# Performance work log

Hardware: AMD Instinct MI355X
Metric: run time of the kernel (lower is better)

## Reference

```python
import jax, jax.numpy as jnp
import numpy as np

B, S, D = 4, 2048, 1024
H, HD = 16, 64  # n_heads, head_dim (n_kv_heads == n_heads -> n_rep = 1)
WINDOW = 256
ROPE_THETA = 10000.0


def setup_inputs() -> dict:
    key = jax.random.key(0)
    ks = jax.random.split(key, 5)
    x = jax.random.normal(ks[0], (B, S, D), dtype=jnp.float32)
    scale = 0.02
    wq = jax.random.normal(ks[1], (D, D), dtype=jnp.float32) * scale
    wk = jax.random.normal(ks[2], (D, D), dtype=jnp.float32) * scale
    wv = jax.random.normal(ks[3], (D, D), dtype=jnp.float32) * scale
    wo = jax.random.normal(ks[4], (D, D), dtype=jnp.float32) * scale
    # RoPE frequencies: freqs_cis[t, i] = exp(1j * t / theta^(2i/HD)), i in [0, HD/2)
    inv_freq = 1.0 / (ROPE_THETA ** (jnp.arange(0, HD, 2, dtype=jnp.float32) / HD))
    t = jnp.arange(S, dtype=jnp.float32)
    ang = t[:, None] * inv_freq[None, :]  # [S, HD/2]
    return {"x": x, "freqs_cos": jnp.cos(ang), "freqs_sin": jnp.sin(ang),
            "wq": wq, "wk": wk, "wv": wv, "wo": wo}


def _apply_rope(xq, xk, cos, sin):
    # xq/xk: [B, S, H, HD]; cos/sin: [S, HD/2] broadcast as [1, S, 1, HD/2]
    def rot(v):
        vr = v.reshape(*v.shape[:-1], HD // 2, 2)
        v0, v1 = vr[..., 0], vr[..., 1]
        c = cos[None, :, None, :]
        s = sin[None, :, None, :]
        o0 = v0 * c - v1 * s
        o1 = v0 * s + v1 * c
        return jnp.stack([o0, o1], axis=-1).reshape(v.shape)
    return rot(xq), rot(xk)


def reference(x, freqs_cos, freqs_sin, wq, wk, wv, wo):
    b, s, _ = x.shape
    xq = (x @ wq.T).reshape(b, s, H, HD)
    xk = (x @ wk.T).reshape(b, s, H, HD)
    xv = (x @ wv.T).reshape(b, s, H, HD)
    xq, xk = _apply_rope(xq, xk, freqs_cos, freqs_sin)
    # [B, H, S, S] scores
    scores = jnp.einsum('bqhd,bkhd->bhqk', xq, xk) / jnp.sqrt(jnp.float32(HD))
    pos = jnp.arange(s)
    # masked (disallowed) when j > i (future) or i - j >= window
    bad = (pos[None, :] > pos[:, None]) | (pos[:, None] - pos[None, :] >= WINDOW)
    scores = jnp.where(bad[None, None], -jnp.inf, scores)
    attn = jax.nn.softmax(scores.astype(jnp.float32), axis=-1).astype(xq.dtype)
    out = jnp.einsum('bhqk,bkhd->bqhd', attn, xv).reshape(b, s, H * HD)
    return out @ wo.T
```

## Files before the change

### kernel.cpp

```cpp
#include <hip/hip_runtime.h>
#include <hip/hip_bf16.h>


typedef __bf16 bf16_t;
typedef __attribute__((ext_vector_type(8))) __bf16 bf16x8;
typedef __attribute__((ext_vector_type(4))) __bf16 bf16x4;
typedef __attribute__((ext_vector_type(4))) float f32x4;

#define MFMA16(a, b, c) __builtin_amdgcn_mfma_f32_16x16x32_bf16((a), (b), (c), 0, 0, 0)

__device__ __forceinline__ void async16(const void* g, void* l) {
    __builtin_amdgcn_global_load_lds(
        (const __attribute__((address_space(1))) unsigned int*)g,
        (__attribute__((address_space(3))) unsigned int*)l, 16, 0, 0);
}

#define BAR() do { asm volatile("" ::: "memory"); __builtin_amdgcn_s_barrier(); \
                   asm volatile("" ::: "memory"); } while (0)
#define VMC(N) asm volatile("s_waitcnt vmcnt(" #N ")" ::: "memory")

__global__ __launch_bounds__(256) void cvt_all(const float* __restrict__ x,
                                               const float* __restrict__ wq,
                                               const float* __restrict__ wk,
                                               const float* __restrict__ wv,
                                               const float* __restrict__ wo,
                                               bf16_t* __restrict__ xbf,
                                               bf16_t* __restrict__ wqkv,
                                               bf16_t* __restrict__ wobf) {
    const int blk = blockIdx.x;
    const float* s;
    bf16_t* d;
    int base;
    if (blk < 4096)      { s = x;  d = xbf;            base = blk; }
    else if (blk < 4608) { s = wq; d = wqkv;           base = blk - 4096; }
    else if (blk < 5120) { s = wk; d = wqkv + 1048576; base = blk - 4608; }
    else if (blk < 5632) { s = wv; d = wqkv + 2097152; base = blk - 5120; }
    else                 { s = wo; d = wobf;           base = blk - 5632; }
    const int i = (base * 256 + threadIdx.x) * 8;
    float4 a = *(const float4*)(s + i);
    float4 b = *(const float4*)(s + i + 4);
    bf16x8 o;
    o[0] = (bf16_t)a.x; o[1] = (bf16_t)a.y; o[2] = (bf16_t)a.z; o[3] = (bf16_t)a.w;
    o[4] = (bf16_t)b.x; o[5] = (bf16_t)b.y; o[6] = (bf16_t)b.z; o[7] = (bf16_t)b.w;
    *(bf16x8*)(d + i) = o;
}

template <typename OUT>
__global__ __launch_bounds__(512, 1) __attribute__((amdgpu_waves_per_eu(2)))
void gemm192(const bf16_t* __restrict__ A, const bf16_t* __restrict__ Bw,
             OUT* __restrict__ C, int M, int N, int K) {
    __shared__ __attribute__((aligned(16))) bf16_t As[32768];
    __shared__ __attribute__((aligned(16))) bf16_t Bs[24576];
    const int tid = threadIdx.x;
    const int l = tid & 63, w = tid >> 6;
    const int lr = l & 15, lg = l >> 4;
    const int wr = w >> 2, wc = w & 3;

    const int nwg = gridDim.x * gridDim.y;
    const int flat = blockIdx.y * gridDim.x + blockIdx.x;
    const int swz = (flat & 7) * (nwg >> 3) + (flat >> 3);
    const int bx = swz % gridDim.x, by = swz / gridDim.x;
    const long m0 = (long)by * 256, n0 = (long)bx * 192;
    const int NT = K >> 6;
    const int NI = NT >> 1;

    const int p  = w * 1024 + l * 16;
    const int pp = p ^ (((p >> 9) & 1) << 5);
    const int st = pp >> 10;
    const int rSt = (st >> 1) * 16 + ((pp >> 6) & 15);
    const int cSt = (st & 1) * 32 + ((pp >> 4) & 3) * 8;
    const bf16_t* aS = A  + (m0 + rSt) * K + cSt;
    const bf16_t* bS = Bw + (n0 + rSt) * K + cSt;
    const long uK = 64L * K;

    auto stageA = [&](int b, int u, int t) {
        async16(aS + (long)u * uK + (long)t * 64,
                (char*)As + b * 32768 + u * 8192 + w * 1024);
    };
    auto stageB = [&](int b, int u, int t) {
        async16(bS + (long)u * uK + (long)t * 64,
                (char*)Bs + b * 24576 + u * 8192 + w * 1024);
    };

    f32x4 acc[8][3] = {};
    bf16x8 afX[4], afY[4], bfX[3], bfY[3];
    const int swd = (lr & 8) << 2;

    auto loadAF = [&](int b, int mh, int ks, bf16x8 (&dst)[4]) {
#pragma unroll
        for (int mi = 0; mi < 4; ++mi) {
            const int off = (wr * 2 + mh) * 8192 + (mi * 2 + ks) * 1024 +
                            lr * 64 + lg * 16;
            dst[mi] = *(const bf16x8*)((const char*)As + b * 32768 + (off ^ swd));
        }
    };
    auto loadBF = [&](int b, int ks, bf16x8 (&dst)[3]) {
#pragma unroll
        for (int nj = 0; nj < 3; ++nj) {
            const int rg = wc * 48 + nj * 16 + lr;
            const int off = (rg >> 6) * 8192 + (((rg >> 4) & 3) * 2 + ks) * 1024 +
                            lr * 64 + lg * 16;
            dst[nj] = *(const bf16x8*)((const char*)Bs + b * 24576 + (off ^ swd));
        }
    };

#define QMM(MH, AF, BF) do {                                                   \
    __builtin_amdgcn_s_setprio(1);                                             \
    _Pragma("unroll")                                                          \
    for (int mi = 0; mi < 4; ++mi)                                             \
        _Pragma("unroll")                                                      \
        for (int nj = 0; nj < 3; ++nj)                                         \
            acc[(MH)*4+mi][nj] = MFMA16((AF)[mi], (BF)[nj], acc[(MH)*4+mi][nj]); \
    __builtin_amdgcn_s_setprio(0);                                             \
} while (0)

    stageA(0, 0, 0); stageA(0, 1, 0); stageA(0, 2, 0); stageA(0, 3, 0);
    stageB(0, 0, 0); stageB(0, 1, 0); stageB(0, 2, 0);
    stageB(1, 0, 1); stageB(1, 1, 1); stageB(1, 2, 1);
    VMC(3);
    BAR();

#pragma unroll 1
    for (int it = 0; it < NI - 1; ++it) {
        const int T = 2 * it;
        loadAF(0, 0, 0, afX); loadBF(0, 0, bfX);
        stageA(1, 0, T + 1); stageA(1, 1, T + 1);
        BAR(); QMM(0, afX, bfX); BAR();
        loadAF(0, 1, 0, afY);
        stageA(1, 2, T + 1); stageA(1, 3, T + 1);
        BAR(); QMM(1, afY, bfX); BAR();
        loadAF(0, 0, 1, afX); loadBF(0, 1, bfY);
        BAR(); QMM(0, afX, bfY); BAR();
        loadAF(0, 1, 1, afY);
        stageB(0, 0, T + 2);
        BAR(); QMM(1, afY, bfY); VMC(1); BAR();
        loadAF(1, 0, 0, afX); loadBF(1, 0, bfX);
        stageB(0, 1, T + 2); stageB(0, 2, T + 2);
        BAR(); QMM(0, afX, bfX); BAR();
        loadAF(1, 1, 0, afY);
        stageA(0, 0, T + 2); stageA(0, 1, T + 2);
        BAR(); QMM(1, afY, bfX); BAR();
        loadAF(1, 0, 1, afX); loadBF(1, 1, bfY);
        stageA(0, 2, T + 2); stageA(0, 3, T + 2);
        BAR(); QMM(0, afX, bfY); BAR();
        loadAF(1, 1, 1, afY);
        stageB(1, 0, T + 3); stageB(1, 1, T + 3); stageB(1, 2, T + 3);
        BAR(); QMM(1, afY, bfY); VMC(3); BAR();
    }

    {
        loadAF(0, 0, 0, afX); loadBF(0, 0, bfX);
        stageA(1, 0, NT - 1); stageA(1, 1, NT - 1);
        BAR(); QMM(0, afX, bfX); BAR();
        loadAF(0, 1, 0, afY);
        stageA(1, 2, NT - 1); stageA(1, 3, NT - 1);
        BAR(); QMM(1, afY, bfX); BAR();
        loadAF(0, 0, 1, afX); loadBF(0, 1, bfY);
        BAR(); QMM(0, afX, bfY); BAR();
        loadAF(0, 1, 1, afY);
        BAR(); QMM(1, afY, bfY);
        VMC(0); BAR();
        loadAF(1, 0, 0, afX); loadBF(1, 0, bfX);
        QMM(0, afX, bfX);
        loadAF(1, 1, 0, afY);
        QMM(1, afY, bfX);
        loadAF(1, 0, 1, afX); loadBF(1, 1, bfY);
        QMM(0, afX, bfY);
        loadAF(1, 1, 1, afY);
        QMM(1, afY, bfY);
    }
#undef QMM

#pragma unroll
    for (int ai = 0; ai < 8; ++ai)
#pragma unroll
        for (int nj = 0; nj < 3; ++nj)
#pragma unroll
            for (int j = 0; j < 4; ++j) {
                long r = m0 + wr * 128 + ai * 16 + lg * 4 + j;
                long c = n0 + wc * 48 + nj * 16 + lr;
                C[r * (long)N + c] = (OUT)acc[ai][nj][j];
            }
}

template <typename OUT>
__global__ __launch_bounds__(512, 2) void gemm256(const bf16_t* __restrict__ A,
                                                  const bf16_t* __restrict__ Bw,
                                                  OUT* __restrict__ C,
                                                  int M, int N, int K) {
    __shared__ __attribute__((aligned(16))) bf16_t As[49152];
    __shared__ __attribute__((aligned(16))) bf16_t Bs[24576];
    const int tid = threadIdx.x;
    const int l = tid & 63, w = tid >> 6;
    const int lr = l & 15, lg = l >> 4;
    const int wr = w >> 1, wc = w & 1;

    const int nwg = gridDim.x * gridDim.y;
    const int flat = blockIdx.y * gridDim.x + blockIdx.x;
    const int swz = (flat & 7) * (nwg >> 3) + (flat >> 3);
    const int bx = swz % gridDim.x, by = swz / gridDim.x;
    const long m0 = (long)by * 256, n0 = (long)bx * 128;
    const int NT = K >> 6;

    int rS[2], cS[2];
#pragma unroll
    for (int i = 0; i < 2; ++i) {
        const int p  = i * 8192 + w * 1024 + l * 16;
        const int pp = p ^ (((p >> 9) & 1) << 5);
        const int st = pp >> 10;
        rS[i] = (st >> 1) * 16 + ((pp >> 6) & 15);
        cS[i] = (st & 1) * 32 + ((pp >> 4) & 3) * 8;
    }
    const bf16_t* aSrc0 = A  + (m0 + rS[0]) * K + cS[0];
    const bf16_t* aSrc1 = A  + (m0 + rS[1]) * K + cS[1];
    const bf16_t* bSrc0 = Bw + (n0 + rS[0]) * K + cS[0];
    const bf16_t* bSrc1 = Bw + (n0 + rS[1]) * K + cS[1];
    const long hK = 128L * K;

    auto stageA = [&](int b, int h, int t) {
        char* d = (char*)As + b * 32768 + h * 16384 + w * 1024;
        const long o = (long)h * hK + (long)t * 64;
        async16(aSrc0 + o, d);
        async16(aSrc1 + o, d + 8192);
    };
    auto stageB = [&](int b, int t) {
        char* d = (char*)Bs + b * 16384 + w * 1024;
        const long o = (long)t * 64;
        async16(bSrc0 + o, d);
        async16(bSrc1 + o, d + 8192);
    };

    f32x4 acc[4][4] = {};
    bf16x8 af[4][2], blo[2][2], bhi[2][2];
    const int swd = (lr & 8) << 2;

    auto loadA = [&](int b) {
#pragma unroll
        for (int mi = 0; mi < 4; ++mi)
#pragma unroll
            for (int ks = 0; ks < 2; ++ks) {
                const int ra = (wr & 1) * 64 + mi * 16 + lr;
                const int off = ((ra >> 4) * 2 + ks) * 1024 + (ra & 15) * 64 + lg * 16;
                af[mi][ks] = *(const bf16x8*)((const char*)As + b * 32768 +
                                              (wr >> 1) * 16384 + (off ^ swd));
            }
    };
    auto loadB = [&](int b, int nh, bf16x8 (&dst)[2][2]) {
#pragma unroll
        for (int nj = 0; nj < 2; ++nj)
#pragma unroll
            for (int ks = 0; ks < 2; ++ks) {
                const int rb = wc * 64 + (nh * 2 + nj) * 16 + lr;
                const int off = ((rb >> 4) * 2 + ks) * 1024 + (rb & 15) * 64 + lg * 16;
                dst[nj][ks] = *(const bf16x8*)((const char*)Bs + b * 16384 +
                                               (off ^ swd));
            }
    };

#define QMM(NH, BF) do {                                                       \
    __builtin_amdgcn_s_setprio(1);                                             \
    _Pragma("unroll")                                                          \
    for (int mi = 0; mi < 4; ++mi) {                                           \
        acc[mi][(NH)*2]   = MFMA16(af[mi][0], (BF)[0][0], acc[mi][(NH)*2]);    \
        acc[mi][(NH)*2]   = MFMA16(af[mi][1], (BF)[0][1], acc[mi][(NH)*2]);    \
        acc[mi][(NH)*2+1] = MFMA16(af[mi][0], (BF)[1][0], acc[mi][(NH)*2+1]);  \
        acc[mi][(NH)*2+1] = MFMA16(af[mi][1], (BF)[1][1], acc[mi][(NH)*2+1]);  \
    }                                                                          \
    __builtin_amdgcn_s_setprio(0);                                             \
} while (0)

    stageA(0, 0, 0); stageA(0, 1, 0); stageB(0, 0);
    stageA(1, 0, 1); stageA(1, 1, 1); stageB(1, 1);
    VMC(6);
    BAR();

    int bc = 0;
#pragma unroll 1
    for (int t = 0; t < NT - 2; ++t) {
        const int bn = (bc + 2 >= 3) ? bc - 1 : bc + 2;
        loadA(bc); loadB(bc, 0, blo); stageA(bn, 0, t + 2); stageA(bn, 1, t + 2);
        BAR(); QMM(0, blo); BAR();
        loadB(bc, 1, bhi); stageB(bn, t + 2);
        BAR(); QMM(1, bhi);
        if (t < NT - 3) { VMC(6); } else { VMC(0); }
        BAR();
        bc = (bc + 1 >= 3) ? 0 : bc + 1;
    }
    {
        loadA(bc); loadB(bc, 0, blo);
        QMM(0, blo);
        loadB(bc, 1, bhi);
        QMM(1, bhi);
        const int b2 = (bc + 1 >= 3) ? 0 : bc + 1;
        loadA(b2); loadB(b2, 0, blo);
        QMM(0, blo);
        loadB(b2, 1, bhi);
        QMM(1, bhi);
    }
#undef QMM

#pragma unroll
    for (int mi = 0; mi < 4; ++mi)
#pragma unroll
        for (int ni = 0; ni < 4; ++ni)
#pragma unroll
            for (int j = 0; j < 4; ++j) {
                long r = m0 + wr * 64 + mi * 16 + lg * 4 + j;
                long c = n0 + wc * 64 + ni * 16 + lr;
                C[r * N + c] = (OUT)acc[mi][ni][j];
            }
}

__global__ __launch_bounds__(256) void rope_reshape(const bf16_t* __restrict__ Cq,
                                                    const float* __restrict__ fcos,
                                                    const float* __restrict__ fsin,
                                                    bf16_t* __restrict__ Qo,
                                                    bf16_t* __restrict__ Ko,
                                                    bf16_t* __restrict__ VT) {
    __shared__ __attribute__((aligned(16))) bf16_t vt[64][72];
    const int blk = blockIdx.x;
    const int st = blk & 31, bh = blk >> 5;
    const int h = bh & 15, b = bh >> 4;
    const int s0 = st << 6;
    const int tid = threadIdx.x;
    const int i = tid >> 2, dq = (tid & 3) << 4;
    const int s = s0 + i;

    const bf16_t* base = Cq + (long)(b * 2048 + s) * 3072 + h * 64 + dq;
    bf16x8 q0v = *(const bf16x8*)(base);
    bf16x8 q1v = *(const bf16x8*)(base + 8);
    bf16x8 k0v = *(const bf16x8*)(base + 1024);
    bf16x8 k1v = *(const bf16x8*)(base + 1032);
    bf16x8 v0v = *(const bf16x8*)(base + 2048);
    bf16x8 v1v = *(const bf16x8*)(base + 2056);

    float cs[8], sn[8];
    {
        const float* cp = fcos + (long)s * 32 + (dq >> 1);
        const float* sp = fsin + (long)s * 32 + (dq >> 1);
        float4 a = *(const float4*)cp, b2 = *(const float4*)(cp + 4);
        float4 c = *(const float4*)sp, d2 = *(const float4*)(sp + 4);
        cs[0]=a.x; cs[1]=a.y; cs[2]=a.z; cs[3]=a.w; cs[4]=b2.x; cs[5]=b2.y; cs[6]=b2.z; cs[7]=b2.w;
        sn[0]=c.x; sn[1]=c.y; sn[2]=c.z; sn[3]=c.w; sn[4]=d2.x; sn[5]=d2.y; sn[6]=d2.z; sn[7]=d2.w;
    }

    auto rope8 = [&](bf16x8 v, int fo) -> bf16x8 {
        bf16x8 o;
#pragma unroll
        for (int p = 0; p < 4; ++p) {
            float v0 = (float)v[2 * p], v1 = (float)v[2 * p + 1];
            float c = cs[fo + p], s2 = sn[fo + p];
            o[2 * p]     = (bf16_t)(v0 * c - v1 * s2);
            o[2 * p + 1] = (bf16_t)(v0 * s2 + v1 * c);
        }
        return o;
    };

    bf16x8 qo0 = rope8(q0v, 0), qo1 = rope8(q1v, 4);
    bf16x8 ko0 = rope8(k0v, 0), ko1 = rope8(k1v, 4);

    const long qaddr = ((long)bh * 2048 + s) * 64 + dq;
    *(bf16x8*)(Qo + qaddr) = qo0;
    *(bf16x8*)(Qo + qaddr + 8) = qo1;
    *(bf16x8*)(Ko + qaddr) = ko0;
    *(bf16x8*)(Ko + qaddr + 8) = ko1;

    *(bf16x8*)&vt[i][dq] = v0v;
    *(bf16x8*)&vt[i][dq + 8] = v1v;
    __syncthreads();
    const int d = tid >> 2, sb = (tid & 3) << 4;
    bf16x8 o0, o1;
#pragma unroll
    for (int j = 0; j < 8; ++j) {
        const int f = ((j & 3) << 1) | ((j >> 2) & 1);
        o0[j] = vt[sb + f][d];
        o1[j] = vt[sb + 8 + f][d];
    }
    const long va = ((long)bh * 64 + d) * 2048 + s0 + sb;
    *(bf16x8*)(VT + va) = o0;
    *(bf16x8*)(VT + va + 8) = o1;
}

__global__ __launch_bounds__(256, 2) void attn_win4(const bf16_t* __restrict__ Q,
                                                    const bf16_t* __restrict__ Kb,
                                                    const bf16_t* __restrict__ VT,
                                                    bf16_t* __restrict__ Ao) {
    __shared__ __attribute__((aligned(16))) bf16_t kld[5 * 4096];
    __shared__ __attribute__((aligned(16))) bf16_t vld[5 * 4096];
    const int raw = blockIdx.x;
    const int mswz = ((raw & 7) << 8) | (raw >> 3);
    const int qt = mswz & 31, bh = mswz >> 5;
    const int h = bh & 15, b = bh >> 4;
    const int l = threadIdx.x & 63, w = threadIdx.x >> 6;
    const int lr = l & 15, lg = l >> 4;
    const int q0 = qt * 64 + w * 16;
    const int q = q0 + lr;
    const int tb = qt - 4;

    const bf16_t* Qp = Q + (long)bh * 2048 * 64;
    const bf16_t* Kp = Kb + (long)bh * 2048 * 64;
    const bf16_t* Vp = VT + (long)bh * 64 * 2048;

#pragma unroll
    for (int u = 0; u < 5; ++u) {
        const int kt = tb + u;
        const int kt64 = (kt < 0 ? 0 : kt) * 64;
#pragma unroll
        for (int part = 0; part < 2; ++part) {
            const int seg = w * 2 + part;
            const int r = seg * 8 + (l >> 3);
            const int sc = (l & 7) ^ ((r >> 1) & 7);
            async16(Kp + (long)(kt64 + r) * 64 + sc * 8,
                    (char*)kld + u * 8192 + seg * 1024);
            async16(Vp + (long)r * 2048 + kt64 + sc * 8,
                    (char*)vld + u * 8192 + seg * 1024);
        }
    }

    const bf16x8 qb0 = *(const bf16x8*)&Qp[q * 64 + lg * 8];
    const bf16x8 qb1 = *(const bf16x8*)&Qp[q * 64 + 32 + lg * 8];

    __syncthreads();

    float mrun = -1000.f, lsum = 0.f;
    f32x4 o0 = {0.f, 0.f, 0.f, 0.f}, o1 = {0.f, 0.f, 0.f, 0.f};
    f32x4 o2 = {0.f, 0.f, 0.f, 0.f}, o3 = {0.f, 0.f, 0.f, 0.f};
    const int swv = (lr >> 1) & 7;

    const char* kbase;
    const char* vbase;
    int k0s;

#define QKCORE(HH, MM)                                                           \
        const int row_ = (HH) * 32 + 2 * lr + (MM);                              \
        const int sw_ = (row_ >> 1) & 7;                                         \
        bf16x8 k0_ = *(const bf16x8*)(kbase + row_ * 128 + ((lg ^ sw_) << 4));   \
        bf16x8 k1_ = *(const bf16x8*)(kbase + row_ * 128 + (((4 + lg) ^ sw_) << 4)); \
        f32x4 s_ = {0.f, 0.f, 0.f, 0.f};                                         \
        s_ = MFMA16(k0_, qb0, s_);                                               \
        s_ = MFMA16(k1_, qb1, s_);

#define QKF_F(DST, HH, MM)                                                       \
    f32x4 DST; { QKCORE(HH, MM)                                                  \
        const int kb_ = k0s + (HH) * 32 + (MM) + lg * 8;                         \
        DST[0] = ((kb_ >= 0) & ((unsigned)(q - kb_) < 256u))         ? s_[0] * 0.125f : -1e30f; \
        DST[1] = ((kb_ + 2 >= 0) & ((unsigned)(q - kb_ - 2) < 256u)) ? s_[1] * 0.125f : -1e30f; \
        DST[2] = ((kb_ + 4 >= 0) & ((unsigned)(q - kb_ - 4) < 256u)) ? s_[2] * 0.125f : -1e30f; \
        DST[3] = ((kb_ + 6 >= 0) & ((unsigned)(q - kb_ - 6) < 256u)) ? s_[3] * 0.125f : -1e30f; \
    }

#define QKF_U(DST, HH, MM)                                                       \
    f32x4 DST; { QKCORE(HH, MM)                                                  \
        const int d_ = q - (k0s + (HH) * 32 + (MM) + lg * 8);                    \
        DST[0] = (d_ < 256)     ? s_[0] * 0.125f : -1e30f;                       \
        DST[1] = (d_ - 2 < 256) ? s_[1] * 0.125f : -1e30f;                       \
        DST[2] = (d_ - 4 < 256) ? s_[2] * 0.125f : -1e30f;                       \
        DST[3] = (d_ - 6 < 256) ? s_[3] * 0.125f : -1e30f;                       \
    }

#define QKF_L(DST, HH, MM)                                                       \
    f32x4 DST; { QKCORE(HH, MM)                                                  \
        const int d_ = q - (k0s + (HH) * 32 + (MM) + lg * 8);                    \
        DST[0] = (d_ >= 0)     ? s_[0] * 0.125f : -1e30f;                        \
        DST[1] = (d_ - 2 >= 0) ? s_[1] * 0.125f : -1e30f;                        \
        DST[2] = (d_ - 4 >= 0) ? s_[2] * 0.125f : -1e30f;                        \
        DST[3] = (d_ - 6 >= 0) ? s_[3] * 0.125f : -1e30f;                        \
    }

#define QKF_N(DST, HH, MM)                                                       \
    f32x4 DST; { QKCORE(HH, MM)                                                  \
        DST[0] = s_[0] * 0.125f; DST[1] = s_[1] * 0.125f;                        \
        DST[2] = s_[2] * 0.125f; DST[3] = s_[3] * 0.125f;                        \
    }

#define EXV(S_) {                                                                \
        S_[0] = __expf(S_[0] - mnew); S_[1] = __expf(S_[1] - mnew);              \
        S_[2] = __expf(S_[2] - mnew); S_[3] = __expf(S_[3] - mnew);              \
        rs += (S_[0] + S_[1]) + (S_[2] + S_[3]); }

#define PVF(NT, HH, PB) {                                                        \
        bf16x8 va_ = *(const bf16x8*)(vbase + ((NT) * 16 + lr) * 128 +           \
                                      ((((HH) * 4 + lg) ^ swv) << 4));           \
        o##NT = MFMA16(va_, PB, o##NT); }

#define TILEBODY(QKM) {                                                          \
        QKM(sA, 0, 0) QKM(sB, 0, 1) QKM(sC, 1, 0) QKM(sD, 1, 1)                  \
        float tm = fmaxf(fmaxf(fmaxf(sA[0], sA[1]), fmaxf(sA[2], sA[3])),        \
                         fmaxf(fmaxf(sB[0], sB[1]), fmaxf(sB[2], sB[3])));       \
        tm = fmaxf(tm, fmaxf(fmaxf(fmaxf(sC[0], sC[1]), fmaxf(sC[2], sC[3])),    \
                             fmaxf(fmaxf(sD[0], sD[1]), fmaxf(sD[2], sD[3]))));  \
        tm = fmaxf(tm, __shfl_xor(tm, 16));                                      \
        tm = fmaxf(tm, __shfl_xor(tm, 32));                                      \
        const float mnew = fmaxf(mrun, tm);                                      \
        const float alpha = __expf(mrun - mnew);                                 \
        mrun = mnew;                                                             \
        float rs = 0.f;                                                          \
        EXV(sA) EXV(sB) EXV(sC) EXV(sD)                                          \
        rs += __shfl_xor(rs, 16);                                                \
        rs += __shfl_xor(rs, 32);                                                \
        lsum = lsum * alpha + rs;                                                \
        o0[0] *= alpha; o0[1] *= alpha; o0[2] *= alpha; o0[3] *= alpha;          \
        o1[0] *= alpha; o1[1] *= alpha; o1[2] *= alpha; o1[3] *= alpha;          \
        o2[0] *= alpha; o2[1] *= alpha; o2[2] *= alpha; o2[3] *= alpha;          \
        o3[0] *= alpha; o3[1] *= alpha; o3[2] *= alpha; o3[3] *= alpha;          \
        bf16x8 pb0, pb1;                                                         \
        pb0[0] = (bf16_t)sA[0]; pb0[1] = (bf16_t)sA[1]; pb0[2] = (bf16_t)sA[2]; pb0[3] = (bf16_t)sA[3]; \
        pb0[4] = (bf16_t)sB[0]; pb0[5] = (bf16_t)sB[1]; pb0[6] = (bf16_t)sB[2]; pb0[7] = (bf16_t)sB[3]; \
        pb1[0] = (bf16_t)sC[0]; pb1[1] = (bf16_t)sC[1]; pb1[2] = (bf16_t)sC[2]; pb1[3] = (bf16_t)sC[3]; \
        pb1[4] = (bf16_t)sD[0]; pb1[5] = (bf16_t)sD[1]; pb1[6] = (bf16_t)sD[2]; pb1[7] = (bf16_t)sD[3]; \
        PVF(0, 0, pb0) PVF(1, 0, pb0) PVF(2, 0, pb0) PVF(3, 0, pb0)              \
        PVF(0, 1, pb1) PVF(1, 1, pb1) PVF(2, 1, pb1) PVF(3, 1, pb1)              \
    }

#define SETT(U) kbase = (const char*)kld + (U) * 8192;                           \
                vbase = (const char*)vld + (U) * 8192;                           \
                k0s = (tb + (U)) * 64;

    if (qt >= 4) {
        SETT(0) TILEBODY(QKF_U)
        SETT(1) TILEBODY(QKF_N)
        SETT(2) TILEBODY(QKF_N)
        SETT(3) TILEBODY(QKF_N)
        SETT(4) TILEBODY(QKF_L)
    } else {
#pragma unroll
        for (int u = 0; u < 5; ++u) {
            SETT(u) TILEBODY(QKF_F)
        }
    }
#undef SETT
#undef TILEBODY
#undef QKF_F
#undef QKF_U
#undef QKF_L
#undef QKF_N
#undef QKCORE
#undef EXV
#undef PVF

    const float rinv = 1.0f / lsum;
    bf16_t* aor = Ao + ((long)(b * 2048) + q) * 1024 + h * 64;
#define EPI(NT, OA_) {                                                           \
        bf16x4 ov_;                                                             \
        ov_[0] = (bf16_t)(OA_[0] * rinv); ov_[1] = (bf16_t)(OA_[1] * rinv);      \
        ov_[2] = (bf16_t)(OA_[2] * rinv); ov_[3] = (bf16_t)(OA_[3] * rinv);      \
        *(bf16x4*)(aor + (NT) * 16 + lg * 4) = ov_; }
    EPI(0, o0) EPI(1, o1) EPI(2, o2) EPI(3, o3)
#undef EPI
}

extern "C" void kernel_launch(void* const* d_in, const int* in_sizes, int n_in,
                              void* d_out, int out_size, void* d_ws, size_t ws_size,
                              hipStream_t stream) {
    (void)in_sizes; (void)n_in; (void)out_size; (void)ws_size;
    const float* x    = (const float*)d_in[0];
    const float* fcos = (const float*)d_in[1];
    const float* fsin = (const float*)d_in[2];
    const float* wq   = (const float*)d_in[3];
    const float* wk   = (const float*)d_in[4];
    const float* wv   = (const float*)d_in[5];
    const float* wo   = (const float*)d_in[6];
    float* out = (float*)d_out;

    char* ws = (char*)d_ws;
    bf16_t* xbf  = (bf16_t*)(ws);
    bf16_t* wqkv = (bf16_t*)(ws + 16777216);
    bf16_t* wobf = (bf16_t*)(ws + 23068672);
    bf16_t* qkvc = (bf16_t*)(ws + 25165824);
    bf16_t* kbuf = (bf16_t*)(ws + 75497472);
    bf16_t* vtb  = (bf16_t*)(ws + 92274688);
    bf16_t* qbuf = xbf;
    bf16_t* aob  = qkvc;

    cvt_all<<<6144, 256, 0, stream>>>(x, wq, wk, wv, wo, xbf, wqkv, wobf);

    gemm192<bf16_t><<<dim3(16, 32), 512, 0, stream>>>(xbf, wqkv, qkvc, 8192, 3072, 1024);
    rope_reshape<<<2048, 256, 0, stream>>>(qkvc, fcos, fsin, qbuf, kbuf, vtb);
    attn_win4<<<2048, 256, 0, stream>>>(qbuf, kbuf, vtb, aob);
    gemm256<float><<<dim3(8, 32), 512, 0, stream>>>(aob, wobf, out, 8192, 1024, 1024);
}
```

Before: 133.9 us.

## Fuse RoPE and Q/K head reshape into QKV GEMM epilogue

The QKV GEMM epilogue now applies RoPE to the Q and K columns, using a lane shuffle to fetch the paired element, and writes them straight into head-major Q/K buffers. The V columns go to a separate temporary buffer, and a smaller transpose kernel then produces V^T. This drops the round trip of the Q and K parts of the QKV intermediate through global memory. In exchange, the epilogue does scalar scattered bf16 stores and per-element cos/sin loads, which may coalesce poorly and lengthen the GEMM tail.

```diff
diff --git a/kernel.cpp b/kernel.cpp
--- a/kernel.cpp
+++ b/kernel.cpp
@@ -45,10 +45,11 @@
     *(bf16x8*)(d + i) = o;
 }
 
-template <typename OUT>
 __global__ __launch_bounds__(512, 1) __attribute__((amdgpu_waves_per_eu(2)))
-void gemm192(const bf16_t* __restrict__ A, const bf16_t* __restrict__ Bw,
-             OUT* __restrict__ C, int M, int N, int K) {
+void gemm192_qkv(const bf16_t* __restrict__ A, const bf16_t* __restrict__ Bw,
+                 const float* __restrict__ fcos, const float* __restrict__ fsin,
+                 bf16_t* __restrict__ Qo, bf16_t* __restrict__ Ko,
+                 bf16_t* __restrict__ Vtmp, int M, int N, int K) {
     __shared__ __attribute__((aligned(16))) bf16_t As[32768];
     __shared__ __attribute__((aligned(16))) bf16_t Bs[24576];
     const int tid = threadIdx.x;
@@ -172,15 +173,72 @@
 #undef QMM
 
 #pragma unroll
-    for (int ai = 0; ai < 8; ++ai)
-#pragma unroll
-        for (int nj = 0; nj < 3; ++nj)
-#pragma unroll
-            for (int j = 0; j < 4; ++j) {
-                long r = m0 + wr * 128 + ai * 16 + lg * 4 + j;
-                long c = n0 + wc * 48 + nj * 16 + lr;
-                C[r * (long)N + c] = (OUT)acc[ai][nj][j];
-            }
+    for (int nj = 0; nj < 3; ++nj) {
+        const int cbase = (int)n0 + wc * 48 + nj * 16;
+        const int cls = cbase >> 10;
+        const int c = cbase + lr;
+        if (cls == 2) {
+            bf16_t* vp = Vtmp + (c - 2048);
+#pragma unroll
+            for (int ai = 0; ai < 8; ++ai)
+#pragma unroll
+                for (int j = 0; j < 4; ++j) {
+                    const long t = m0 + wr * 128 + ai * 16 + lg * 4 + j;
+                    vp[t * 1024] = (bf16_t)acc[ai][nj][j];
+                }
+        } else {
+            const int d = c & 63;
+            const int p2 = d >> 1;
+            const int h = (c >> 6) & 15;
+            const float sgn = (lr & 1) ? 1.f : -1.f;
+            bf16_t* qk = (cls == 0) ? Qo : Ko;
+#pragma unroll
+            for (int ai = 0; ai < 8; ++ai)
+#pragma unroll
+                for (int j = 0; j < 4; ++j) {
+                    const long t = m0 + wr * 128 + ai * 16 + lg * 4 + j;
+                    const int s = (int)(t & 2047);
+                    const int bb = (int)(t >> 11);
+                    const float v = acc[ai][nj][j];
+                    const float pv = __shfl_xor(v, 1);
+                    const float cc = fcos[s * 32 + p2];
+                    const float ss = fsin[s * 32 + p2];
+                    const float o = v * cc + sgn * (pv * ss);
+                    qk[((long)(bb * 16 + h) * 2048 + s) * 64 + d] = (bf16_t)o;
+                }
+        }
+    }
+}
+
+__global__ __launch_bounds__(256) void vt_transpose(const bf16_t* __restrict__ V,
+                                                    bf16_t* __restrict__ VT) {
+    __shared__ __attribute__((aligned(16))) bf16_t vt[64][72];
+    const int blk = blockIdx.x;
+    const int st = blk & 31, bh = blk >> 5;
+    const int h = bh & 15, b = bh >> 4;
+    const int s0 = st << 6;
+    const int tid = threadIdx.x;
+    const int i = tid >> 2, dq = (tid & 3) << 4;
+    const int s = s0 + i;
+
+    const bf16_t* base = V + (long)(b * 2048 + s) * 1024 + h * 64 + dq;
+    bf16x8 v0v = *(const bf16x8*)(base);
+    bf16x8 v1v = *(const bf16x8*)(base + 8);
+
+    *(bf16x8*)&vt[i][dq] = v0v;
+    *(bf16x8*)&vt[i][dq + 8] = v1v;
+    __syncthreads();
+    const int d = tid >> 2, sb = (tid & 3) << 4;
+    bf16x8 o0, o1;
+#pragma unroll
+    for (int j = 0; j < 8; ++j) {
+        const int f = ((j & 3) << 1) | ((j >> 2) & 1);
+        o0[j] = vt[sb + f][d];
+        o1[j] = vt[sb + 8 + f][d];
+    }
+    const long va = ((long)bh * 64 + d) * 2048 + s0 + sb;
+    *(bf16x8*)(VT + va) = o0;
+    *(bf16x8*)(VT + va + 8) = o1;
 }
 
 template <typename OUT>
@@ -309,76 +367,6 @@
                 long c = n0 + wc * 64 + ni * 16 + lr;
                 C[r * N + c] = (OUT)acc[mi][ni][j];
             }
-}
-
-__global__ __launch_bounds__(256) void rope_reshape(const bf16_t* __restrict__ Cq,
-                                                    const float* __restrict__ fcos,
-                                                    const float* __restrict__ fsin,
-                                                    bf16_t* __restrict__ Qo,
-                                                    bf16_t* __restrict__ Ko,
-                                                    bf16_t* __restrict__ VT) {
-    __shared__ __attribute__((aligned(16))) bf16_t vt[64][72];
-    const int blk = blockIdx.x;
-    const int st = blk & 31, bh = blk >> 5;
-    const int h = bh & 15, b = bh >> 4;
-    const int s0 = st << 6;
-    const int tid = threadIdx.x;
-    const int i = tid >> 2, dq = (tid & 3) << 4;
-    const int s = s0 + i;
-
-    const bf16_t* base = Cq + (long)(b * 2048 + s) * 3072 + h * 64 + dq;
-    bf16x8 q0v = *(const bf16x8*)(base);
-    bf16x8 q1v = *(const bf16x8*)(base + 8);
-    bf16x8 k0v = *(const bf16x8*)(base + 1024);
-    bf16x8 k1v = *(const bf16x8*)(base + 1032);
-    bf16x8 v0v = *(const bf16x8*)(base + 2048);
-    bf16x8 v1v = *(const bf16x8*)(base + 2056);
-
-    float cs[8], sn[8];
-    {
-        const float* cp = fcos + (long)s * 32 + (dq >> 1);
-        const float* sp = fsin + (long)s * 32 + (dq >> 1);
-        float4 a = *(const float4*)cp, b2 = *(const float4*)(cp + 4);
-        float4 c = *(const float4*)sp, d2 = *(const float4*)(sp + 4);
-        cs[0]=a.x; cs[1]=a.y; cs[2]=a.z; cs[3]=a.w; cs[4]=b2.x; cs[5]=b2.y; cs[6]=b2.z; cs[7]=b2.w;
-        sn[0]=c.x; sn[1]=c.y; sn[2]=c.z; sn[3]=c.w; sn[4]=d2.x; sn[5]=d2.y; sn[6]=d2.z; sn[7]=d2.w;
-    }
-
-    auto rope8 = [&](bf16x8 v, int fo) -> bf16x8 {
-        bf16x8 o;
-#pragma unroll
-        for (int p = 0; p < 4; ++p) {
-            float v0 = (float)v[2 * p], v1 = (float)v[2 * p + 1];
-            float c = cs[fo + p], s2 = sn[fo + p];
-            o[2 * p]     = (bf16_t)(v0 * c - v1 * s2);
-            o[2 * p + 1] = (bf16_t)(v0 * s2 + v1 * c);
-        }
-        return o;
-    };
-
-    bf16x8 qo0 = rope8(q0v, 0), qo1 = rope8(q1v, 4);
-    bf16x8 ko0 = rope8(k0v, 0), ko1 = rope8(k1v, 4);
-
-    const long qaddr = ((long)bh * 2048 + s) * 64 + dq;
-    *(bf16x8*)(Qo + qaddr) = qo0;
-    *(bf16x8*)(Qo + qaddr + 8) = qo1;
-    *(bf16x8*)(Ko + qaddr) = ko0;
-    *(bf16x8*)(Ko + qaddr + 8) = ko1;
-
-    *(bf16x8*)&vt[i][dq] = v0v;
-    *(bf16x8*)&vt[i][dq + 8] = v1v;
-    __syncthreads();
-    const int d = tid >> 2, sb = (tid & 3) << 4;
-    bf16x8 o0, o1;
-#pragma unroll
-    for (int j = 0; j < 8; ++j) {
-        const int f = ((j & 3) << 1) | ((j >> 2) & 1);
-        o0[j] = vt[sb + f][d];
-        o1[j] = vt[sb + 8 + f][d];
-    }
-    const long va = ((long)bh * 64 + d) * 2048 + s0 + sb;
-    *(bf16x8*)(VT + va) = o0;
-    *(bf16x8*)(VT + va + 8) = o1;
 }
 
 __global__ __launch_bounds__(256, 2) void attn_win4(const bf16_t* __restrict__ Q,
@@ -566,16 +554,18 @@
     bf16_t* xbf  = (bf16_t*)(ws);
     bf16_t* wqkv = (bf16_t*)(ws + 16777216);
     bf16_t* wobf = (bf16_t*)(ws + 23068672);
-    bf16_t* qkvc = (bf16_t*)(ws + 25165824);
+    bf16_t* vtmp = (bf16_t*)(ws + 25165824);
+    bf16_t* qbuf = (bf16_t*)(ws + 41943040);
     bf16_t* kbuf = (bf16_t*)(ws + 75497472);
     bf16_t* vtb  = (bf16_t*)(ws + 92274688);
-    bf16_t* qbuf = xbf;
-    bf16_t* aob  = qkvc;
+    bf16_t* aob  = xbf;
 
     cvt_all<<<6144, 256, 0, stream>>>(x, wq, wk, wv, wo, xbf, wqkv, wobf);
 
-    gemm192<bf16_t><<<dim3(16, 32), 512, 0, stream>>>(xbf, wqkv, qkvc, 8192, 3072, 1024);
-    rope_reshape<<<2048, 256, 0, stream>>>(qkvc, fcos, fsin, qbuf, kbuf, vtb);
+    gemm192_qkv<<<dim3(16, 32), 512, 0, stream>>>(xbf, wqkv, fcos, fsin,
+                                                  qbuf, kbuf, vtmp,
+                                                  8192, 3072, 1024);
+    vt_transpose<<<2048, 256, 0, stream>>>(vtmp, vtb);
     attn_win4<<<2048, 256, 0, stream>>>(qbuf, kbuf, vtb, aob);
     gemm256<float><<<dim3(8, 32), 512, 0, stream>>>(aob, wobf, out, 8192, 1024, 1024);
 }
```

New measurement: 130.1 us. -2.9%, faster.
